# Kernel tuning notes

Hardware: AMD Instinct MI355X
Metric: run time of the kernel (lower is better)

Reference implementation:

```python
import jax, jax.numpy as jnp
import numpy as np
import math

VOCAB, DIM, N_LAYERS, N_HEADS, SEQ, BATCH = 32000, 768, 4, 12, 2048, 1
HEAD_DIM = DIM // N_HEADS
HIDDEN = int(DIM * 2.66)  # 2042
THETA = 10000.0


def setup_inputs() -> dict:
    key = jax.random.key(0)
    ks = jax.random.split(key, 14)
    s = 0.02
    return {
        "tokens": jax.random.randint(ks[0], (BATCH, SEQ), 0, VOCAB),
        "emb": jax.random.normal(ks[1], (VOCAB, DIM), jnp.float32) * s,
        "wq": jax.random.normal(ks[2], (N_LAYERS, DIM, DIM), jnp.float32) * s,
        "wk": jax.random.normal(ks[3], (N_LAYERS, DIM, DIM), jnp.float32) * s,
        "wv": jax.random.normal(ks[4], (N_LAYERS, DIM, DIM), jnp.float32) * s,
        "wo": jax.random.normal(ks[5], (N_LAYERS, DIM, DIM), jnp.float32) * s,
        "w1": jax.random.normal(ks[6], (N_LAYERS, HIDDEN, DIM), jnp.float32) * s,
        "w2": jax.random.normal(ks[7], (N_LAYERS, DIM, HIDDEN), jnp.float32) * s,
        "w3": jax.random.normal(ks[8], (N_LAYERS, HIDDEN, DIM), jnp.float32) * s,
        "attn_norm_w": jnp.ones((N_LAYERS, DIM), jnp.float32),
        "ffn_norm_w": jnp.ones((N_LAYERS, DIM), jnp.float32),
        "norm_w": jnp.ones((DIM,), jnp.float32),
        "out_w": jax.random.normal(ks[9], (VOCAB, DIM), jnp.float32) * s,
    }


def rmsnorm(x, w, eps=1e-6):
    return x * jax.lax.rsqrt(jnp.mean(x * x, axis=-1, keepdims=True) + eps) * w


def rope_tables(seqlen):
    freqs = 1.0 / (THETA ** (jnp.arange(0, HEAD_DIM, 2, dtype=jnp.float32) / HEAD_DIM))
    ang = jnp.arange(seqlen, dtype=jnp.float32)[:, None] * freqs[None, :]  # [S, hd/2]
    return jnp.cos(ang)[None, :, None, :], jnp.sin(ang)[None, :, None, :]


def apply_rope(x, cos, sin):
    # x: [B,S,H,hd]; complex rotation on consecutive pairs
    xr = x.reshape(*x.shape[:-1], HEAD_DIM // 2, 2)
    a, b = xr[..., 0], xr[..., 1]
    out = jnp.stack([a * cos - b * sin, a * sin + b * cos], axis=-1)
    return out.reshape(x.shape)


def reference(tokens, emb, wq, wk, wv, wo, w1, w2, w3, attn_norm_w, ffn_norm_w, norm_w, out_w):
    B, S = tokens.shape
    h = emb[tokens]  # [B,S,D]
    cos, sin = rope_tables(S)
    mask = jnp.triu(jnp.full((S, S), -jnp.inf, jnp.float32), k=1)  # causal
    scale = 1.0 / math.sqrt(HEAD_DIM)
    for i in range(N_LAYERS):
        x = rmsnorm(h, attn_norm_w[i])
        q = (x @ wq[i].T).reshape(B, S, N_HEADS, HEAD_DIM)
        k = (x @ wk[i].T).reshape(B, S, N_HEADS, HEAD_DIM)
        v = (x @ wv[i].T).reshape(B, S, N_HEADS, HEAD_DIM)
        q = apply_rope(q, cos, sin)
        k = apply_rope(k, cos, sin)
        scores = jnp.einsum("bqhd,bkhd->bhqk", q, k) * scale + mask
        p = jax.nn.softmax(scores, axis=-1)
        o = jnp.einsum("bhqk,bkhd->bqhd", p, v).reshape(B, S, DIM)
        h = h + o @ wo[i].T
        y = rmsnorm(h, ffn_norm_w[i])
        h = h + (jax.nn.silu(y @ w1[i].T) * (y @ w3[i].T)) @ w2[i].T
    h = rmsnorm(h, norm_w)
    logits = h @ out_w.T  # [B,S,V]
    return logits
```

## Files before the change

kernel.cpp:

```cpp
#include <hip/hip_runtime.h>
#include <math.h>

typedef unsigned int uint32;
typedef unsigned short ushort_t;

typedef __attribute__((ext_vector_type(8))) short short8;
typedef __attribute__((ext_vector_type(4))) float floatx4;

#define SEQL 2048
#define DIMC 768
#define NHEAD 12
#define HDIM 64
#define HIDV 2042
#define HIDP 2048
#define NVOCAB 32000
#define QKS 1536
#define QSZ (DIMC*DIMC)
#define PSZ (HIDP*DIMC)
#define W2SRC (DIMC*HIDV)

__device__ __forceinline__ ushort_t f2bf(float f) {
    uint32 u = __float_as_uint(f);
    u += 0x7FFFu + ((u >> 16) & 1u);
    return (ushort_t)(u >> 16);
}
__device__ __forceinline__ float bf2f(ushort_t h) {
    return __uint_as_float(((uint32)h) << 16);
}

union Frag { short8 s8; uint32 u[4]; ushort_t us[8]; };

#define GLOAD_LDS16(g, l) \
    __builtin_amdgcn_global_load_lds((const __attribute__((address_space(1))) void*)(g), \
                                     (__attribute__((address_space(3))) void*)(l), 16, 0, 0)

template<int BM, int BN, int OUTMODE>
__global__ __launch_bounds__(256)
void gemm_lds_kernel(const ushort_t* __restrict__ A, int lda,
                     const ushort_t* __restrict__ B, int ldb,
                     void* __restrict__ C, int ldc, int K)
{
    constexpr int WTM = BM / 32;
    constexpr int WTN = BN / 32;
    __shared__ __align__(16) ushort_t As[2][BM * 32];
    __shared__ __align__(16) ushort_t Bs[2][BN * 32];

    const int tid = threadIdx.x;
    const int nwg  = gridDim.x * gridDim.y;
    const int lid0 = blockIdx.y * gridDim.x + blockIdx.x;
    const int lid  = (lid0 & 7) * (nwg >> 3) + (lid0 >> 3);
    const int bx = lid % gridDim.x;
    const int by = lid / gridDim.x;

    const int wid = tid >> 6, lane = tid & 63;
    const int wm = wid & 1, wn = wid >> 1;
    const int r = lane & 15, quad = lane >> 4;
    const int m0 = bx * BM;
    const int n0 = by * BN;

    floatx4 acc[WTM][WTN];
#pragma unroll
    for (int i = 0; i < WTM; ++i)
#pragma unroll
        for (int j = 0; j < WTN; ++j) acc[i][j] = (floatx4){0.f, 0.f, 0.f, 0.f};

    const int row_a = tid >> 2;
    const int col8  = (tid & 3) * 8;
    const ushort_t* gA = A + (size_t)(m0 + row_a) * lda + col8;
    const ushort_t* gB = B + (size_t)(n0 + row_a) * ldb + col8;

    auto stage = [&](int buf, int k0) {
        GLOAD_LDS16(gA + k0, &As[buf][(size_t)tid * 8]);
        if (BM == 128) GLOAD_LDS16(gA + (size_t)64 * lda + k0, &As[buf][(size_t)(tid + 256) * 8]);
        GLOAD_LDS16(gB + k0, &Bs[buf][(size_t)tid * 8]);
        if (BN == 128) GLOAD_LDS16(gB + (size_t)64 * ldb + k0, &Bs[buf][(size_t)(tid + 256) * 8]);
    };

    stage(0, 0);
    __syncthreads();
    int buf = 0;
    for (int k0 = 0; k0 < K; k0 += 32) {
        if (k0 + 32 < K) stage(buf ^ 1, k0 + 32);
        const ushort_t* pa = &As[buf][(wm * (BM / 2) + r) * 32 + quad * 8];
        const ushort_t* pb = &Bs[buf][(wn * (BN / 2) + r) * 32 + quad * 8];
        short8 af[WTM], bf[WTN];
#pragma unroll
        for (int i = 0; i < WTM; ++i) af[i] = *(const short8*)(pa + i * 16 * 32);
#pragma unroll
        for (int j = 0; j < WTN; ++j) bf[j] = *(const short8*)(pb + j * 16 * 32);
#pragma unroll
        for (int i = 0; i < WTM; ++i)
#pragma unroll
            for (int j = 0; j < WTN; ++j)
                acc[i][j] = __builtin_amdgcn_mfma_f32_16x16x32_bf16(af[i], bf[j], acc[i][j], 0, 0, 0);
        __syncthreads();
        buf ^= 1;
    }

#pragma unroll
    for (int i = 0; i < WTM; ++i) {
        const int row = m0 + wm * (BM / 2) + i * 16 + quad * 4;
#pragma unroll
        for (int j = 0; j < WTN; ++j) {
            const int col = n0 + wn * (BN / 2) + j * 16 + r;
#pragma unroll
            for (int t = 0; t < 4; ++t) {
                const size_t off = (size_t)(row + t) * ldc + col;
                const float v = acc[i][j][t];
                if (OUTMODE == 2)      ((float*)C)[off] += v;
                else if (OUTMODE == 1) ((ushort_t*)C)[off] = f2bf(v);
                else                   ((float*)C)[off] = v;
            }
        }
    }
}

__global__ __launch_bounds__(256)
void rmsnorm_kernel(const float* __restrict__ x, const float* __restrict__ g,
                    ushort_t* __restrict__ out)
{
    const int w = threadIdx.x >> 6, lane = threadIdx.x & 63;
    const int row = blockIdx.x * 4 + w;
    const float* xr = x + (size_t)row * DIMC;
    float4 a = *(const float4*)(xr + lane * 4);
    float4 b = *(const float4*)(xr + 256 + lane * 4);
    float4 c = *(const float4*)(xr + 512 + lane * 4);
    float ss = a.x*a.x + a.y*a.y + a.z*a.z + a.w*a.w
             + b.x*b.x + b.y*b.y + b.z*b.z + b.w*b.w
             + c.x*c.x + c.y*c.y + c.z*c.z + c.w*c.w;
#pragma unroll
    for (int off = 32; off > 0; off >>= 1) ss += __shfl_xor(ss, off, 64);
    const float inv = rsqrtf(ss * (1.0f / DIMC) + 1e-6f);
    float4 ga = *(const float4*)(g + lane * 4);
    float4 gb = *(const float4*)(g + 256 + lane * 4);
    float4 gc = *(const float4*)(g + 512 + lane * 4);
    ushort_t* orow = out + (size_t)row * DIMC;
    *(ushort4*)(orow + lane * 4)       = make_ushort4(f2bf(a.x*inv*ga.x), f2bf(a.y*inv*ga.y), f2bf(a.z*inv*ga.z), f2bf(a.w*inv*ga.w));
    *(ushort4*)(orow + 256 + lane * 4) = make_ushort4(f2bf(b.x*inv*gb.x), f2bf(b.y*inv*gb.y), f2bf(b.z*inv*gb.z), f2bf(b.w*inv*gb.w));
    *(ushort4*)(orow + 512 + lane * 4) = make_ushort4(f2bf(c.x*inv*gc.x), f2bf(c.y*inv*gc.y), f2bf(c.z*inv*gc.z), f2bf(c.w*inv*gc.w));
}

__global__ __launch_bounds__(256)
void rope_kernel(ushort_t* __restrict__ x)
{
    const int idx = blockIdx.x * 256 + threadIdx.x;
    const int j = idx & 31;
    const int h = (idx >> 5) % 24;
    const int s = idx / 768;
    const float freq = expf(-0.28782313662425574f * (float)j);
    const float ang = (float)s * freq;
    const float sn = sinf(ang), cs = cosf(ang);
    ushort_t* p = x + (size_t)s * QKS + h * HDIM + 2 * j;
    const float a = bf2f(p[0]), b = bf2f(p[1]);
    p[0] = f2bf(a * cs - b * sn);
    p[1] = f2bf(a * sn + b * cs);
}

__global__ __launch_bounds__(256)
void attn_mfma_kernel(const ushort_t* __restrict__ Q, const ushort_t* __restrict__ K,
                      const ushort_t* __restrict__ VT, ushort_t* __restrict__ O,
                      int qks)
{
    __shared__ __align__(16) ushort_t Ks[2][64 * 64];
    __shared__ __align__(16) ushort_t Vs[2][64 * 64];

    const int tid = threadIdx.x;
    const int w = tid >> 6, lane = tid & 63;
    const int r = lane & 15, quad = lane >> 4;
    const int hb = blockIdx.y * HDIM;
    const int bx = 31 - (int)blockIdx.x;
    const int qb = bx * 64 + w * 16;
    const int nit = bx + 1;

    const int c_row = tid >> 3;
    const int c_col = ((tid & 7) ^ (c_row & 7)) << 3;
    const int swz = (r & 7) << 4;

    Frag bq[2];
    {
        const ushort_t* qp = Q + (size_t)(qb + r) * qks + hb + quad * 8;
#pragma unroll
        for (int fi = 0; fi < 2; ++fi) {
            Frag t; t.s8 = *(const short8*)(qp + fi * 32);
#pragma unroll
            for (int e = 0; e < 8; ++e) t.us[e] = f2bf(bf2f(t.us[e]) * 0.125f);
            bq[fi] = t;
        }
    }

    floatx4 o[4];
#pragma unroll
    for (int dg = 0; dg < 4; ++dg) o[dg] = (floatx4){0.f, 0.f, 0.f, 0.f};
    float m = -INFINITY, l = 0.f;

    auto stage = [&](int buf, int kc) {
        const ushort_t* kg = K + (size_t)(kc + c_row) * qks + hb + c_col;
        GLOAD_LDS16(kg,                      &Ks[buf][(size_t)tid * 8]);
        GLOAD_LDS16(kg + (size_t)32 * qks,   &Ks[buf][(size_t)(tid + 256) * 8]);
        const ushort_t* vg = VT + (size_t)(hb + c_row) * SEQL + kc + c_col;
        GLOAD_LDS16(vg,                      &Vs[buf][(size_t)tid * 8]);
        GLOAD_LDS16(vg + (size_t)32 * SEQL,  &Vs[buf][(size_t)(tid + 256) * 8]);
    };

    stage(0, 0);
    __syncthreads();

    for (int it = 0; it < nit; ++it) {
        const int buf = it & 1;
        const int kc = it * 64;
        if (it + 1 < nit) stage(buf ^ 1, kc + 64);

        const char* ksb = (const char*)Ks[buf];
        const char* vsb = (const char*)Vs[buf];

        floatx4 st[4];
#pragma unroll
        for (int s = 0; s < 4; ++s) {
            st[s] = (floatx4){0.f, 0.f, 0.f, 0.f};
#pragma unroll
            for (int f = 0; f < 2; ++f) {
                const int lb = (s * 16 + r) * 128 + ((f * 64 + quad * 16) ^ swz);
                const short8 a = *(const short8*)(ksb + lb);
                st[s] = __builtin_amdgcn_mfma_f32_16x16x32_bf16(a, bq[f].s8, st[s], 0, 0, 0);
            }
        }

        if (it == nit - 1) {
            const int q = qb + r;
#pragma unroll
            for (int s = 0; s < 4; ++s)
#pragma unroll
                for (int tt = 0; tt < 4; ++tt)
                    if (kc + s * 16 + quad * 4 + tt > q) st[s][tt] = -INFINITY;
        }

        float vm = -INFINITY;
#pragma unroll
        for (int s = 0; s < 4; ++s)
            vm = fmaxf(vm, fmaxf(fmaxf(st[s][0], st[s][1]), fmaxf(st[s][2], st[s][3])));
        vm = fmaxf(vm, __shfl_xor(vm, 16, 64));
        vm = fmaxf(vm, __shfl_xor(vm, 32, 64));
        const float mnew = fmaxf(m, vm);
        const float alpha = __expf(m - mnew);
        float p[4][4];
        float ps = 0.f;
#pragma unroll
        for (int s = 0; s < 4; ++s)
#pragma unroll
            for (int tt = 0; tt < 4; ++tt) {
                p[s][tt] = __expf(st[s][tt] - mnew);
                ps += p[s][tt];
            }
        ps += __shfl_xor(ps, 16, 64);
        ps += __shfl_xor(ps, 32, 64);
        l = l * alpha + ps;
        m = mnew;

        Frag ap0, ap1;
        ap0.u[0] = (uint32)f2bf(p[0][0]) | ((uint32)f2bf(p[0][1]) << 16);
        ap0.u[1] = (uint32)f2bf(p[0][2]) | ((uint32)f2bf(p[0][3]) << 16);
        ap0.u[2] = (uint32)f2bf(p[1][0]) | ((uint32)f2bf(p[1][1]) << 16);
        ap0.u[3] = (uint32)f2bf(p[1][2]) | ((uint32)f2bf(p[1][3]) << 16);
        ap1.u[0] = (uint32)f2bf(p[2][0]) | ((uint32)f2bf(p[2][1]) << 16);
        ap1.u[1] = (uint32)f2bf(p[2][2]) | ((uint32)f2bf(p[2][3]) << 16);
        ap1.u[2] = (uint32)f2bf(p[3][0]) | ((uint32)f2bf(p[3][1]) << 16);
        ap1.u[3] = (uint32)f2bf(p[3][2]) | ((uint32)f2bf(p[3][3]) << 16);

#pragma unroll
        for (int dg = 0; dg < 4; ++dg) {
            const int rowb = (dg * 16 + r) * 128;
            Frag av0, av1;
            *(uint2*)&av0.u[0] = *(const uint2*)(vsb + rowb + ((quad * 8) ^ swz));
            *(uint2*)&av0.u[2] = *(const uint2*)(vsb + rowb + ((32 + quad * 8) ^ swz));
            *(uint2*)&av1.u[0] = *(const uint2*)(vsb + rowb + ((64 + quad * 8) ^ swz));
            *(uint2*)&av1.u[2] = *(const uint2*)(vsb + rowb + ((96 + quad * 8) ^ swz));
            o[dg] *= alpha;
            o[dg] = __builtin_amdgcn_mfma_f32_16x16x32_bf16(av0.s8, ap0.s8, o[dg], 0, 0, 0);
            o[dg] = __builtin_amdgcn_mfma_f32_16x16x32_bf16(av1.s8, ap1.s8, o[dg], 0, 0, 0);
        }

        __syncthreads();
    }

    const float inv = 1.0f / l;
    ushort_t* op = O + (size_t)(qb + r) * DIMC + hb + quad * 4;
#pragma unroll
    for (int dg = 0; dg < 4; ++dg) {
        uint2 pkd;
        pkd.x = (uint32)f2bf(o[dg][0] * inv) | ((uint32)f2bf(o[dg][1] * inv) << 16);
        pkd.y = (uint32)f2bf(o[dg][2] * inv) | ((uint32)f2bf(o[dg][3] * inv) << 16);
        *(uint2*)(op + dg * 16) = pkd;
    }
}

__global__ __launch_bounds__(256)
void silu_mul_kernel(const float* __restrict__ y13, ushort_t* __restrict__ hs)
{
    const int idx = blockIdx.x * 256 + threadIdx.x;
    const int s = idx >> 9;
    const int c = (idx & 511) * 4;
    const float* row = y13 + (size_t)s * 4096;
    float4 a = *(const float4*)(row + c);
    float4 b = *(const float4*)(row + 2048 + c);
    float4 r;
    r.x = a.x / (1.f + __expf(-a.x)) * b.x;
    r.y = a.y / (1.f + __expf(-a.y)) * b.y;
    r.z = a.z / (1.f + __expf(-a.z)) * b.z;
    r.w = a.w / (1.f + __expf(-a.w)) * b.w;
    *(ushort4*)(hs + (size_t)s * HIDP + c) = make_ushort4(f2bf(r.x), f2bf(r.y), f2bf(r.z), f2bf(r.w));
}

__global__ __launch_bounds__(256)
void embed_kernel(const int* __restrict__ tok, const float* __restrict__ emb,
                  float* __restrict__ h)
{
    const int idx = blockIdx.x * 256 + threadIdx.x;
    const int s = idx / 192, c = (idx % 192) * 4;
    const int t = tok[s];
    *(float4*)(h + (size_t)s * DIMC + c) = *(const float4*)(emb + (size_t)t * DIMC + c);
}

__global__ __launch_bounds__(256)
void conv_layer_kernel(const float* __restrict__ wq, const float* __restrict__ wk,
                       const float* __restrict__ wv, const float* __restrict__ wo,
                       const float* __restrict__ w1, const float* __restrict__ w2,
                       const float* __restrict__ w3,
                       ushort_t* __restrict__ wqb, ushort_t* __restrict__ wkb,
                       ushort_t* __restrict__ wvb, ushort_t* __restrict__ wob,
                       ushort_t* __restrict__ w1p, ushort_t* __restrict__ w3p,
                       ushort_t* __restrict__ w2p)
{
    int idx = blockIdx.x * 256 + threadIdx.x;
    if (idx < 4 * QSZ) {
        const int m = idx / QSZ, i = idx - m * QSZ;
        const float* s = (m == 0) ? wq : (m == 1) ? wk : (m == 2) ? wv : wo;
        ushort_t*   d = (m == 0) ? wqb : (m == 1) ? wkb : (m == 2) ? wvb : wob;
        d[i] = f2bf(s[i]);
        return;
    }
    idx -= 4 * QSZ;
    if (idx < PSZ) {
        const int n = idx / DIMC, kk = idx - n * DIMC;
        w1p[idx] = (n < HIDV) ? f2bf(w1[(size_t)n * DIMC + kk]) : (ushort_t)0;
        return;
    }
    idx -= PSZ;
    if (idx < PSZ) {
        const int n = idx / DIMC, kk = idx - n * DIMC;
        w3p[idx] = (n < HIDV) ? f2bf(w3[(size_t)n * DIMC + kk]) : (ushort_t)0;
        return;
    }
    idx -= PSZ;
    if (idx < PSZ) {
        const int n = idx >> 11, kk = idx & 2047;
        w2p[idx] = (kk < HIDV) ? f2bf(w2[(size_t)n * HIDV + kk]) : (ushort_t)0;
        return;
    }
}

__global__ __launch_bounds__(256)
void conv_outw_kernel(const float* __restrict__ src, ushort_t* __restrict__ dst)
{
    const size_t idx = (size_t)(blockIdx.x * 256 + threadIdx.x);
    float4 a = *(const float4*)(src + idx * 4);
    *(ushort4*)(dst + idx * 4) = make_ushort4(f2bf(a.x), f2bf(a.y), f2bf(a.z), f2bf(a.w));
}

extern "C" void kernel_launch(void* const* d_in, const int* in_sizes, int n_in,
                              void* d_out, int out_size, void* d_ws, size_t ws_size,
                              hipStream_t stream)
{
    const int*   tok  = (const int*)d_in[0];
    const float* emb  = (const float*)d_in[1];
    const float* wq   = (const float*)d_in[2];
    const float* wk   = (const float*)d_in[3];
    const float* wv   = (const float*)d_in[4];
    const float* wo   = (const float*)d_in[5];
    const float* w1   = (const float*)d_in[6];
    const float* w2   = (const float*)d_in[7];
    const float* w3   = (const float*)d_in[8];
    const float* anw  = (const float*)d_in[9];
    const float* fnw  = (const float*)d_in[10];
    const float* nw   = (const float*)d_in[11];
    const float* outw = (const float*)d_in[12];
    float* out = (float*)d_out;
    (void)in_sizes; (void)n_in; (void)out_size; (void)ws_size;

    char* p = (char*)d_ws;
    auto alloc = [&](size_t bytes) { char* r = p; p += (bytes + 255) & ~(size_t)255; return r; };
    float*    H   = (float*)   alloc((size_t)SEQL * DIMC * 4);
    ushort_t* XN  = (ushort_t*)alloc((size_t)SEQL * DIMC * 2);
    ushort_t* YN  = (ushort_t*)alloc((size_t)SEQL * DIMC * 2);
    ushort_t* WQB = (ushort_t*)alloc((size_t)QSZ * 2);
    ushort_t* WKB = (ushort_t*)alloc((size_t)QSZ * 2);
    ushort_t* WVB = (ushort_t*)alloc((size_t)QSZ * 2);
    ushort_t* WOB = (ushort_t*)alloc((size_t)QSZ * 2);
    ushort_t* W1P = (ushort_t*)alloc((size_t)PSZ * 2);
    ushort_t* W3P = (ushort_t*)alloc((size_t)PSZ * 2);
    ushort_t* W2P = (ushort_t*)alloc((size_t)PSZ * 2);
    ushort_t* QKB = (ushort_t*)alloc((size_t)SEQL * QKS * 2);
    ushort_t* VTG = (ushort_t*)alloc((size_t)SEQL * DIMC * 2);
    ushort_t* AO  = (ushort_t*)alloc((size_t)SEQL * DIMC * 2);
    float*    Y13 = (float*)   alloc((size_t)SEQL * 4096 * 4);
    ushort_t* HS  = (ushort_t*)alloc((size_t)SEQL * HIDP * 2);
    ushort_t* OUTWB = QKB;

    embed_kernel<<<1536, 256, 0, stream>>>(tok, emb, H);

    for (int l = 0; l < 4; ++l) {
        conv_layer_kernel<<<27648, 256, 0, stream>>>(
            wq + (size_t)l * QSZ, wk + (size_t)l * QSZ, wv + (size_t)l * QSZ, wo + (size_t)l * QSZ,
            w1 + (size_t)l * W2SRC, w2 + (size_t)l * W2SRC, w3 + (size_t)l * W2SRC,
            WQB, WKB, WVB, WOB, W1P, W3P, W2P);

        rmsnorm_kernel<<<512, 256, 0, stream>>>(H, anw + (size_t)l * DIMC, XN);

        gemm_lds_kernel<128,128,1><<<dim3(16,12), 256, 0, stream>>>(XN, DIMC, WQB, DIMC, QKB, QKS, DIMC);
        gemm_lds_kernel<64,128,1><<<dim3(12,16), 256, 0, stream>>>(WVB, DIMC, XN, DIMC, VTG, SEQL, DIMC);

        rope_kernel<<<6144, 256, 0, stream>>>(QKB);

        attn_mfma_kernel<<<dim3(32, NHEAD), 256, 0, stream>>>(QKB, QKB + 768, VTG, AO, QKS);

        gemm_lds_kernel<128,64,2><<<dim3(16,12), 256, 0, stream>>>(AO, DIMC, WOB, DIMC, H, DIMC, DIMC);

        rmsnorm_kernel<<<512, 256, 0, stream>>>(H, fnw + (size_t)l * DIMC, YN);

        gemm_lds_kernel<128,128,0><<<dim3(16,32), 256, 0, stream>>>(YN, DIMC, W1P, DIMC, Y13, 4096, DIMC);

        silu_mul_kernel<<<4096, 256, 0, stream>>>(Y13, HS);

        gemm_lds_kernel<128,64,2><<<dim3(16,12), 256, 0, stream>>>(HS, HIDP, W2P, HIDP, H, DIMC, HIDP);
    }

    rmsnorm_kernel<<<512, 256, 0, stream>>>(H, nw, XN);
    conv_outw_kernel<<<24000, 256, 0, stream>>>(outw, OUTWB);
    gemm_lds_kernel<128,128,0><<<dim3(16,250), 256, 0, stream>>>(XN, DIMC, OUTWB, DIMC, out, NVOCAB, DIMC);
}
```

Baseline: 1.346 ms.

## Widen attention KV tiles to 128 and store W1/W3 GEMM output as bf16

The attention kernel now processes 128 keys per iteration instead of 64, which halves the loop iterations and barriers and doubles the LDS buffers. It also raises wave priority around the MFMA sections. Separately, the W1/W3 GEMM now writes bf16 instead of fp32, and the silu-multiply kernel reads 8 bf16 values per thread, halving that intermediate's memory traffic. The risks are extra masked work on the last causal tile, more registers and LDS use, and lower precision for the pre-activation values.

```diff
diff --git a/kernel.cpp b/kernel.cpp
--- a/kernel.cpp
+++ b/kernel.cpp
@@ -161,8 +161,8 @@
                       const ushort_t* __restrict__ VT, ushort_t* __restrict__ O,
                       int qks)
 {
-    __shared__ __align__(16) ushort_t Ks[2][64 * 64];
-    __shared__ __align__(16) ushort_t Vs[2][64 * 64];
+    __shared__ __align__(16) ushort_t Ks[2][128 * 64];
+    __shared__ __align__(16) ushort_t Vs[2][64 * 128];
 
     const int tid = threadIdx.x;
     const int w = tid >> 6, lane = tid & 63;
@@ -170,10 +170,12 @@
     const int hb = blockIdx.y * HDIM;
     const int bx = 31 - (int)blockIdx.x;
     const int qb = bx * 64 + w * 16;
-    const int nit = bx + 1;
-
-    const int c_row = tid >> 3;
-    const int c_col = ((tid & 7) ^ (c_row & 7)) << 3;
+    const int nit = (bx + 2) >> 1;
+
+    const int krow = tid >> 3;
+    const int kcol = ((tid & 7) ^ (krow & 7)) << 3;
+    const int vrow = tid >> 4;
+    const int vcol = (((tid & 15) ^ (vrow & 7))) << 3;
     const int swz = (r & 7) << 4;
 
     Frag bq[2];
@@ -194,12 +196,16 @@
     float m = -INFINITY, l = 0.f;
 
     auto stage = [&](int buf, int kc) {
-        const ushort_t* kg = K + (size_t)(kc + c_row) * qks + hb + c_col;
+        const ushort_t* kg = K + (size_t)(kc + krow) * qks + hb + kcol;
         GLOAD_LDS16(kg,                      &Ks[buf][(size_t)tid * 8]);
         GLOAD_LDS16(kg + (size_t)32 * qks,   &Ks[buf][(size_t)(tid + 256) * 8]);
-        const ushort_t* vg = VT + (size_t)(hb + c_row) * SEQL + kc + c_col;
+        GLOAD_LDS16(kg + (size_t)64 * qks,   &Ks[buf][(size_t)(tid + 512) * 8]);
+        GLOAD_LDS16(kg + (size_t)96 * qks,   &Ks[buf][(size_t)(tid + 768) * 8]);
+        const ushort_t* vg = VT + (size_t)(hb + vrow) * SEQL + kc + vcol;
         GLOAD_LDS16(vg,                      &Vs[buf][(size_t)tid * 8]);
-        GLOAD_LDS16(vg + (size_t)32 * SEQL,  &Vs[buf][(size_t)(tid + 256) * 8]);
+        GLOAD_LDS16(vg + (size_t)16 * SEQL,  &Vs[buf][(size_t)(tid + 256) * 8]);
+        GLOAD_LDS16(vg + (size_t)32 * SEQL,  &Vs[buf][(size_t)(tid + 512) * 8]);
+        GLOAD_LDS16(vg + (size_t)48 * SEQL,  &Vs[buf][(size_t)(tid + 768) * 8]);
     };
 
     stage(0, 0);
@@ -207,15 +213,16 @@
 
     for (int it = 0; it < nit; ++it) {
         const int buf = it & 1;
-        const int kc = it * 64;
-        if (it + 1 < nit) stage(buf ^ 1, kc + 64);
+        const int kc = it * 128;
+        if (it + 1 < nit) stage(buf ^ 1, kc + 128);
 
         const char* ksb = (const char*)Ks[buf];
         const char* vsb = (const char*)Vs[buf];
 
-        floatx4 st[4];
-#pragma unroll
-        for (int s = 0; s < 4; ++s) {
+        floatx4 st[8];
+        __builtin_amdgcn_s_setprio(1);
+#pragma unroll
+        for (int s = 0; s < 8; ++s) {
             st[s] = (floatx4){0.f, 0.f, 0.f, 0.f};
 #pragma unroll
             for (int f = 0; f < 2; ++f) {
@@ -224,11 +231,12 @@
                 st[s] = __builtin_amdgcn_mfma_f32_16x16x32_bf16(a, bq[f].s8, st[s], 0, 0, 0);
             }
         }
+        __builtin_amdgcn_s_setprio(0);
 
         if (it == nit - 1) {
             const int q = qb + r;
 #pragma unroll
-            for (int s = 0; s < 4; ++s)
+            for (int s = 0; s < 8; ++s)
 #pragma unroll
                 for (int tt = 0; tt < 4; ++tt)
                     if (kc + s * 16 + quad * 4 + tt > q) st[s][tt] = -INFINITY;
@@ -236,48 +244,48 @@
 
         float vm = -INFINITY;
 #pragma unroll
-        for (int s = 0; s < 4; ++s)
+        for (int s = 0; s < 8; ++s)
             vm = fmaxf(vm, fmaxf(fmaxf(st[s][0], st[s][1]), fmaxf(st[s][2], st[s][3])));
         vm = fmaxf(vm, __shfl_xor(vm, 16, 64));
         vm = fmaxf(vm, __shfl_xor(vm, 32, 64));
         const float mnew = fmaxf(m, vm);
         const float alpha = __expf(m - mnew);
-        float p[4][4];
         float ps = 0.f;
 #pragma unroll
-        for (int s = 0; s < 4; ++s)
+        for (int s = 0; s < 8; ++s)
 #pragma unroll
             for (int tt = 0; tt < 4; ++tt) {
-                p[s][tt] = __expf(st[s][tt] - mnew);
-                ps += p[s][tt];
+                st[s][tt] = __expf(st[s][tt] - mnew);
+                ps += st[s][tt];
             }
         ps += __shfl_xor(ps, 16, 64);
         ps += __shfl_xor(ps, 32, 64);
         l = l * alpha + ps;
         m = mnew;
 
-        Frag ap0, ap1;
-        ap0.u[0] = (uint32)f2bf(p[0][0]) | ((uint32)f2bf(p[0][1]) << 16);
-        ap0.u[1] = (uint32)f2bf(p[0][2]) | ((uint32)f2bf(p[0][3]) << 16);
-        ap0.u[2] = (uint32)f2bf(p[1][0]) | ((uint32)f2bf(p[1][1]) << 16);
-        ap0.u[3] = (uint32)f2bf(p[1][2]) | ((uint32)f2bf(p[1][3]) << 16);
-        ap1.u[0] = (uint32)f2bf(p[2][0]) | ((uint32)f2bf(p[2][1]) << 16);
-        ap1.u[1] = (uint32)f2bf(p[2][2]) | ((uint32)f2bf(p[2][3]) << 16);
-        ap1.u[2] = (uint32)f2bf(p[3][0]) | ((uint32)f2bf(p[3][1]) << 16);
-        ap1.u[3] = (uint32)f2bf(p[3][2]) | ((uint32)f2bf(p[3][3]) << 16);
-
+        Frag ap[4];
+#pragma unroll
+        for (int ks = 0; ks < 4; ++ks) {
+            ap[ks].u[0] = (uint32)f2bf(st[2*ks][0])   | ((uint32)f2bf(st[2*ks][1])   << 16);
+            ap[ks].u[1] = (uint32)f2bf(st[2*ks][2])   | ((uint32)f2bf(st[2*ks][3])   << 16);
+            ap[ks].u[2] = (uint32)f2bf(st[2*ks+1][0]) | ((uint32)f2bf(st[2*ks+1][1]) << 16);
+            ap[ks].u[3] = (uint32)f2bf(st[2*ks+1][2]) | ((uint32)f2bf(st[2*ks+1][3]) << 16);
+        }
+
+        __builtin_amdgcn_s_setprio(1);
 #pragma unroll
         for (int dg = 0; dg < 4; ++dg) {
-            const int rowb = (dg * 16 + r) * 128;
-            Frag av0, av1;
-            *(uint2*)&av0.u[0] = *(const uint2*)(vsb + rowb + ((quad * 8) ^ swz));
-            *(uint2*)&av0.u[2] = *(const uint2*)(vsb + rowb + ((32 + quad * 8) ^ swz));
-            *(uint2*)&av1.u[0] = *(const uint2*)(vsb + rowb + ((64 + quad * 8) ^ swz));
-            *(uint2*)&av1.u[2] = *(const uint2*)(vsb + rowb + ((96 + quad * 8) ^ swz));
+            const int rowb = (dg * 16 + r) * 256;
             o[dg] *= alpha;
-            o[dg] = __builtin_amdgcn_mfma_f32_16x16x32_bf16(av0.s8, ap0.s8, o[dg], 0, 0, 0);
-            o[dg] = __builtin_amdgcn_mfma_f32_16x16x32_bf16(av1.s8, ap1.s8, o[dg], 0, 0, 0);
-        }
+#pragma unroll
+            for (int ks = 0; ks < 4; ++ks) {
+                Frag av;
+                *(uint2*)&av.u[0] = *(const uint2*)(vsb + rowb + ((ks * 64 + quad * 8) ^ swz));
+                *(uint2*)&av.u[2] = *(const uint2*)(vsb + rowb + ((ks * 64 + 32 + quad * 8) ^ swz));
+                o[dg] = __builtin_amdgcn_mfma_f32_16x16x32_bf16(av.s8, ap[ks].s8, o[dg], 0, 0, 0);
+            }
+        }
+        __builtin_amdgcn_s_setprio(0);
 
         __syncthreads();
     }
@@ -294,20 +302,25 @@
 }
 
 __global__ __launch_bounds__(256)
-void silu_mul_kernel(const float* __restrict__ y13, ushort_t* __restrict__ hs)
+void silu_mul_kernel(const ushort_t* __restrict__ y13, ushort_t* __restrict__ hs)
 {
     const int idx = blockIdx.x * 256 + threadIdx.x;
-    const int s = idx >> 9;
-    const int c = (idx & 511) * 4;
-    const float* row = y13 + (size_t)s * 4096;
-    float4 a = *(const float4*)(row + c);
-    float4 b = *(const float4*)(row + 2048 + c);
-    float4 r;
-    r.x = a.x / (1.f + __expf(-a.x)) * b.x;
-    r.y = a.y / (1.f + __expf(-a.y)) * b.y;
-    r.z = a.z / (1.f + __expf(-a.z)) * b.z;
-    r.w = a.w / (1.f + __expf(-a.w)) * b.w;
-    *(ushort4*)(hs + (size_t)s * HIDP + c) = make_ushort4(f2bf(r.x), f2bf(r.y), f2bf(r.z), f2bf(r.w));
+    const int s = idx >> 8;
+    const int c = (idx & 255) * 8;
+    const ushort_t* row = y13 + (size_t)s * 4096;
+    short8 a8 = *(const short8*)(row + c);
+    short8 b8 = *(const short8*)(row + 2048 + c);
+    ushort_t ov[8];
+#pragma unroll
+    for (int e = 0; e < 8; ++e) {
+        const float a = bf2f((ushort_t)a8[e]);
+        const float b = bf2f((ushort_t)b8[e]);
+        ov[e] = f2bf(a / (1.f + __expf(-a)) * b);
+    }
+    short8 pk;
+#pragma unroll
+    for (int e = 0; e < 8; ++e) pk[e] = (short)ov[e];
+    *(short8*)(hs + (size_t)s * HIDP + c) = pk;
 }
 
 __global__ __launch_bounds__(256)
@@ -401,7 +414,7 @@
     ushort_t* QKB = (ushort_t*)alloc((size_t)SEQL * QKS * 2);
     ushort_t* VTG = (ushort_t*)alloc((size_t)SEQL * DIMC * 2);
     ushort_t* AO  = (ushort_t*)alloc((size_t)SEQL * DIMC * 2);
-    float*    Y13 = (float*)   alloc((size_t)SEQL * 4096 * 4);
+    ushort_t* Y13 = (ushort_t*)alloc((size_t)SEQL * 4096 * 2);
     ushort_t* HS  = (ushort_t*)alloc((size_t)SEQL * HIDP * 2);
     ushort_t* OUTWB = QKB;
 
@@ -426,9 +439,9 @@
 
         rmsnorm_kernel<<<512, 256, 0, stream>>>(H, fnw + (size_t)l * DIMC, YN);
 
-        gemm_lds_kernel<128,128,0><<<dim3(16,32), 256, 0, stream>>>(YN, DIMC, W1P, DIMC, Y13, 4096, DIMC);
-
-        silu_mul_kernel<<<4096, 256, 0, stream>>>(Y13, HS);
+        gemm_lds_kernel<128,128,1><<<dim3(16,32), 256, 0, stream>>>(YN, DIMC, W1P, DIMC, Y13, 4096, DIMC);
+
+        silu_mul_kernel<<<2048, 256, 0, stream>>>(Y13, HS);
 
         gemm_lds_kernel<128,64,2><<<dim3(16,12), 256, 0, stream>>>(HS, HIDP, W2P, HIDP, H, DIMC, HIDP);
     }
```

Result: faster. 1.305 ms (-3.1%).
